# Optimization experiments

Hardware: AMD Instinct MI355X
Metric: run time of the kernel (lower is better)

## Reference

```python
import jax, jax.numpy as jnp
import numpy as np

EPS = 1e-5

def conv3x3(x, w, b=None):
    # NCHW, OIHW, stride 1, padding 1
    y = jax.lax.conv_general_dilated(x, w, (1, 1), ((1, 1), (1, 1)),
                                     dimension_numbers=('NCHW', 'OIHW', 'NCHW'))
    if b is not None:
        y = y + b[None, :, None, None]
    return y

def batchnorm(x, g, b):
    # training-mode BN (PyTorch default): biased variance over (N,H,W)
    m = x.mean((0, 2, 3), keepdims=True)
    v = x.var((0, 2, 3), keepdims=True)
    return (x - m) * jax.lax.rsqrt(v + EPS) * g[None, :, None, None] + b[None, :, None, None]

def upsample2x_align_corners(x):
    # bilinear, align_corners=True, scale_factor=2
    def lerp_axis(a, Lin, axis):
        Lout = 2 * Lin
        c = jnp.arange(Lout, dtype=a.dtype) * (Lin - 1) / (Lout - 1)
        i0 = jnp.floor(c).astype(jnp.int32)
        i1 = jnp.minimum(i0 + 1, Lin - 1)
        w = c - i0.astype(a.dtype)
        shape = [1] * a.ndim
        shape[axis] = Lout
        w = w.reshape(shape)
        return jnp.take(a, i0, axis=axis) * (1 - w) + jnp.take(a, i1, axis=axis) * w
    x = lerp_axis(x, x.shape[2], 2)
    x = lerp_axis(x, x.shape[3], 3)
    return x

def deform_sample(x, offsets):
    # torchvision DeformConv2d v1 sampling: kernel 3x3, pad 1, offsets [B,18,H,W]
    # layout: per kernel point k (row-major), channels (2k, 2k+1) = (dy, dx)
    B, C, H, W = x.shape
    K = 9
    off = offsets.reshape(B, K, 2, H, W)
    ky, kx = jnp.meshgrid(jnp.arange(3) - 1, jnp.arange(3) - 1, indexing='ij')
    ky = ky.reshape(K).astype(x.dtype)
    kx = kx.reshape(K).astype(x.dtype)
    gy = jnp.arange(H, dtype=x.dtype)[None, None, :, None]
    gx = jnp.arange(W, dtype=x.dtype)[None, None, None, :]
    py = gy + ky[None, :, None, None] + off[:, :, 0]  # [B,K,H,W]
    px = gx + kx[None, :, None, None] + off[:, :, 1]
    y0 = jnp.floor(py)
    x0 = jnp.floor(px)
    wy = (py - y0)[:, None]  # [B,1,K,H,W]
    wx = (px - x0)[:, None]
    y0i = y0.astype(jnp.int32)
    x0i = x0.astype(jnp.int32)
    x_flat = x.reshape(B, C, H * W)
    def gather(yi, xi):
        valid = ((yi >= 0) & (yi < H) & (xi >= 0) & (xi < W))
        idx = jnp.clip(yi, 0, H - 1) * W + jnp.clip(xi, 0, W - 1)  # [B,K,H,W]
        g = jnp.take_along_axis(x_flat, idx.reshape(B, 1, K * H * W), axis=2)
        return g.reshape(B, C, K, H, W) * valid[:, None].astype(x.dtype)
    v00 = gather(y0i, x0i)
    v01 = gather(y0i, x0i + 1)
    v10 = gather(y0i + 1, x0i)
    v11 = gather(y0i + 1, x0i + 1)
    return (v00 * (1 - wy) * (1 - wx) + v01 * (1 - wy) * wx
            + v10 * wy * (1 - wx) + v11 * wy * wx)

def setup_inputs() -> dict:
    key = jax.random.key(0)
    ks = jax.random.split(key, 6)
    B, in_ch, skip_ch, out_ch = 4, 256, 128, 128
    Hs, Ws = 128, 128
    x = jax.random.normal(ks[0], (B, in_ch, Hs // 2, Ws // 2), jnp.float32)
    skip = jax.random.normal(ks[1], (B, skip_ch, Hs, Ws), jnp.float32)
    cat_ch = in_ch + skip_ch
    conv1_w = jax.random.normal(ks[2], (out_ch, cat_ch, 3, 3), jnp.float32) * (2.0 / (cat_ch * 9)) ** 0.5
    off_w = jax.random.normal(ks[3], (18, out_ch, 3, 3), jnp.float32) * 0.01
    off_b = jnp.zeros((18,), jnp.float32)
    def_w = jax.random.normal(ks[4], (out_ch, out_ch, 3, 3), jnp.float32) * (2.0 / (out_ch * 9)) ** 0.5
    def_b = jnp.zeros((out_ch,), jnp.float32)
    return {
        'x': x, 'skip': skip,
        'conv1_w': conv1_w,
        'bn1_g': jnp.ones((out_ch,), jnp.float32), 'bn1_b': jnp.zeros((out_ch,), jnp.float32),
        'off_w': off_w, 'off_b': off_b,
        'def_w': def_w, 'def_b': def_b,
        'bn2_g': jnp.ones((out_ch,), jnp.float32), 'bn2_b': jnp.zeros((out_ch,), jnp.float32),
    }

def reference(x, skip, conv1_w, bn1_g, bn1_b, off_w, off_b, def_w, def_b, bn2_g, bn2_b):
    xu = upsample2x_align_corners(x)
    dh = skip.shape[2] - xu.shape[2]
    dw = skip.shape[3] - xu.shape[3]
    if dh != 0 or dw != 0:
        xu = jnp.pad(xu, ((0, 0), (0, 0), (dh // 2, dh - dh // 2), (dw // 2, dw - dw // 2)))
    cat = jnp.concatenate([skip, xu], axis=1)
    h = jax.nn.relu(batchnorm(conv3x3(cat, conv1_w), bn1_g, bn1_b))
    offsets = conv3x3(h, off_w, off_b)  # [B,18,H,W]
    sampled = deform_sample(h, offsets)  # [B,C,9,H,W]
    O = def_w.shape[0]
    y = jnp.einsum('ock,bckhw->bohw', def_w.reshape(O, def_w.shape[1], 9), sampled)
    y = y + def_b[None, :, None, None]
    return jax.nn.relu(batchnorm(y, bn2_g, bn2_b))
```

## Files before the change

kernel.cpp:

```cpp
#include <hip/hip_runtime.h>
#include <hip/hip_bf16.h>

typedef __hip_bfloat16 bf16;
typedef __bf16 bf16x8 __attribute__((ext_vector_type(8)));
typedef __bf16 bf16x4 __attribute__((ext_vector_type(4)));
typedef float  f32x4  __attribute__((ext_vector_type(4)));

constexpr int NB   = 4;
constexpr int H    = 128;
constexpr int W    = 128;
constexpr int HW   = H * W;
constexpr int NPIX = NB * HW;
constexpr int CCAT = 384;
constexpr int CSKIP= 128;
constexpr int CIN  = 256;
constexpr int CO   = 128;
constexpr int HS   = 64;
constexpr int WP   = 130;
constexpr int K1   = 3456;
constexpr int KD   = 1152;
constexpr int NBORD= 2 * WP + 2 * (WP - 2);
constexpr float EPS = 1e-5f;

__device__ __forceinline__ float b2f(bf16 v){ return __bfloat162float(v); }
__device__ __forceinline__ bf16  f2b(float v){ return __float2bfloat16(v); }

__device__ __forceinline__ void async_copy16(const void* g, void* s){
    __builtin_amdgcn_global_load_lds((const __attribute__((address_space(1))) void*)g,
                                     (__attribute__((address_space(3))) void*)s, 16, 0, 0);
}

__device__ __forceinline__ void border_yx(int p, int& y, int& x){
    if (p < WP)             { y = 0;        x = p; }
    else if (p < 2 * WP)    { y = WP - 1;   x = p - WP; }
    else if (p < 2 * WP + (WP - 2)) { y = p - 2 * WP + 1;          x = 0; }
    else                    { y = p - (2 * WP + (WP - 2)) + 1;     x = WP - 1; }
}

__global__ void k_prep(float* __restrict__ sums, bf16* __restrict__ catp,
                       bf16* __restrict__ hp){
    int i = blockIdx.x * blockDim.x + threadIdx.x;
    int stride = gridDim.x * blockDim.x;
    for (int j = i; j < 512; j += stride) sums[j] = 0.f;
    const int nCat = NB * NBORD * CCAT;
    for (int j = i; j < nCat; j += stride){
        int c = j % CCAT, r = j / CCAT, p = r % NBORD, b = r / NBORD;
        int y, x; border_yx(p, y, x);
        catp[(((size_t)b * WP + y) * WP + x) * CCAT + c] = f2b(0.f);
    }
    const int nHp = NB * NBORD * CO;
    for (int j = i; j < nHp; j += stride){
        int c = j % CO, r = j / CO, p = r % NBORD, b = r / NBORD;
        int y, x; border_yx(p, y, x);
        hp[(((size_t)b * WP + y) * WP + x) * CO + c] = f2b(0.f);
    }
}

__global__ __launch_bounds__(256) void k_build_cat2(const float* __restrict__ x,
                                                    const float* __restrict__ skip,
                                                    bf16* __restrict__ catp){
    constexpr int TS = 66;
    __shared__ bf16 tile[128 * TS];
    int t  = threadIdx.x;
    int y  = blockIdx.x % H, b = blockIdx.x / H;
    int xx = t & 127, cp = t >> 7;

    float cy = (y * 63.0f) / 127.0f;
    int   y0 = (int)cy;
    int   y1 = min(y0 + 1, HS - 1);
    float wy = cy - y0;
    float cxf = (xx * 63.0f) / 127.0f;
    int   x0 = (int)cxf;
    int   x1 = min(x0 + 1, HS - 1);
    float wx = cxf - x0;

    bf16* orow = catp + (((size_t)b * WP + y + 1) * WP + 1) * CCAT;

    for (int chunk = 0; chunk < 6; chunk++){
        int cbase = chunk * 64;
        if (chunk >= 1) __syncthreads();
        if (chunk < 2){
            const float* sb = skip + ((size_t)(b * CSKIP + cbase + cp * 32) * H + y) * W;
#pragma unroll
            for (int i = 0; i < 32; i++)
                tile[xx * TS + cp * 32 + i] = f2b(sb[(size_t)i * HW + xx]);
        } else {
            int icb = (chunk - 2) * 64 + cp * 32;
            const float* xr0 = x + ((size_t)(b * CIN + icb) * HS + y0) * HS;
            const float* xr1 = x + ((size_t)(b * CIN + icb) * HS + y1) * HS;
#pragma unroll
            for (int i = 0; i < 32; i++){
                const float* r0 = xr0 + (size_t)i * HS * HS;
                const float* r1 = xr1 + (size_t)i * HS * HS;
                float v0 = r0[x0] * (1 - wx) + r0[x1] * wx;
                float v1 = r1[x0] * (1 - wx) + r1[x1] * wx;
                tile[xx * TS + cp * 32 + i] = f2b(v0 * (1 - wy) + v1 * wy);
            }
        }
        __syncthreads();
        int cc2 = (t & 31) * 2;
        int px0 = t >> 5;
#pragma unroll
        for (int pp = 0; pp < 16; pp++){
            int px = pp * 8 + px0;
            unsigned int v = *(const unsigned int*)&tile[px * TS + cc2];
            *(unsigned int*)&orow[(size_t)px * CCAT + cbase + cc2] = v;
        }
    }
}

__global__ void k_tr_all(const float* __restrict__ w1, const float* __restrict__ wo,
                         const float* __restrict__ wd,
                         bf16* __restrict__ wt1, bf16* __restrict__ wto,
                         bf16* __restrict__ wtd){
    int i = blockIdx.x * blockDim.x + threadIdx.x;
    if (i < CO * K1){
        int k = i % K1, oc = i / K1;
        int ky = k / 1152, r = k % 1152, kx = r / 384, ic = r % 384;
        wt1[i] = f2b(w1[((oc * CCAT + ic) * 3 + ky) * 3 + kx]);
        return;
    }
    i -= CO * K1;
    if (i < 32 * KD){
        int kk = i % KD, o = i / KD;
        int ky = kk / 384, r = kk % 384, kx = r >> 7, ic = r & 127;
        wto[i] = (o < 18) ? f2b(wo[((o * CO + ic) * 3 + ky) * 3 + kx]) : f2b(0.f);
        return;
    }
    i -= 32 * KD;
    if (i < CO * KD){
        int kk = i % KD, o = i / KD;
        int kp = kk >> 7, c = kk & 127;
        wtd[i] = f2b(wd[(o * CO + c) * 9 + kp]);
    }
}

__global__ __launch_bounds__(256) void k_conv1_mfma(const bf16* __restrict__ catp,
                                                    const bf16* __restrict__ wbt,
                                                    bf16* __restrict__ hp,
                                                    float* __restrict__ sums){
    __shared__ unsigned short Ab[68 * 128];
    __shared__ unsigned short Bb[128 * 64];
    __shared__ float ps[256];
    int t = threadIdx.x;
    int l = t & 63, w = t >> 6;
    int half = blockIdx.x & 1;
    int y = (blockIdx.x >> 1) % H, b = blockIdx.x / (2 * H);
    int px0 = half * 64;

    int pr   = l >> 3;
    int koct = (l & 7) ^ pr;
    int m    = l & 15, quad = l >> 4;
    int wm   = w & 1,  wn   = w >> 1;

    f32x4 acc[2][4];
#pragma unroll
    for (int i = 0; i < 2; i++)
#pragma unroll
        for (int j = 0; j < 4; j++) acc[i][j] = f32x4{0.f, 0.f, 0.f, 0.f};

    const size_t rowStride = (size_t)WP * CCAT;
    for (int ky = 0; ky < 3; ky++){
        const bf16* Arow = catp + ((size_t)(b * WP) + y + ky) * rowStride
                         + (size_t)px0 * CCAT;
        for (int ci = 0; ci < 3; ci++){
            __syncthreads();
            for (int i = w; i < 17; i += 4){
                int G  = i * 64 + l;
                int px = G >> 4, ol = G & 15;
                int osrc = ol ^ (px & 7);
                async_copy16(Arow + (size_t)px * CCAT + ci * 128 + osrc * 8,
                             &Ab[i * 512]);
            }
            for (int kx = 0; kx < 3; kx++){
                for (int s64 = 0; s64 < 2; s64++){
                    if (kx | s64) __syncthreads();
                    int kg = ky * 1152 + kx * 384 + ci * 128 + s64 * 64;
#pragma unroll
                    for (int i = 0; i < 4; i++){
                        int ocg = w * 32 + i * 8;
                        async_copy16(wbt + (size_t)(ocg + pr) * K1 + kg + koct * 8,
                                     &Bb[ocg * 64]);
                    }
                    __syncthreads();
                    const bf16x8* ap = (const bf16x8*)Ab;
                    const bf16x8* bp = (const bf16x8*)Bb;
#pragma unroll
                    for (int ks = 0; ks < 2; ks++){
                        int s = s64 * 2 + ks;
                        bf16x8 af[2], bfr[4];
#pragma unroll
                        for (int mi = 0; mi < 2; mi++){
                            int pxk = wm * 32 + mi * 16 + m + kx;
                            af[mi] = ap[pxk * 16 + ((s * 4 + quad) ^ (pxk & 7))];
                        }
#pragma unroll
                        for (int ni = 0; ni < 4; ni++){
                            int oc = wn * 64 + ni * 16 + m;
                            bfr[ni] = bp[oc * 8 + ((ks * 4 + quad) ^ (oc & 7))];
                        }
#pragma unroll
                        for (int mi = 0; mi < 2; mi++)
#pragma unroll
                            for (int ni = 0; ni < 4; ni++)
                                acc[mi][ni] = __builtin_amdgcn_mfma_f32_16x16x32_bf16(
                                    af[mi], bfr[ni], acc[mi][ni], 0, 0, 0);
                    }
                }
            }
        }
    }
    size_t obase = (((size_t)b * WP + y + 1) * WP + 1 + px0) * CO;
#pragma unroll
    for (int mi = 0; mi < 2; mi++){
        int p0 = wm * 32 + mi * 16 + quad * 4;
#pragma unroll
        for (int ni = 0; ni < 4; ni++){
            int oc = wn * 64 + ni * 16 + m;
#pragma unroll
            for (int r = 0; r < 4; r++)
                hp[obase + (size_t)(p0 + r) * CO + oc] = f2b(acc[mi][ni][r]);
        }
    }
    ps[t] = 0.f;
    __syncthreads();
#pragma unroll
    for (int ni = 0; ni < 4; ni++){
        int ch = wn * 64 + ni * 16 + m;
        float s = 0.f, q = 0.f;
#pragma unroll
        for (int mi = 0; mi < 2; mi++)
#pragma unroll
            for (int r = 0; r < 4; r++){
                float v = acc[mi][ni][r];
                s += v; q += v * v;
            }
        s += __shfl_xor(s, 16); s += __shfl_xor(s, 32);
        q += __shfl_xor(q, 16); q += __shfl_xor(q, 32);
        if (quad == 0){
            atomicAdd(&ps[ch], s);
            atomicAdd(&ps[128 + ch], q);
        }
    }
    __syncthreads();
    if (t < 128){
        atomicAdd(&sums[t],       ps[t]);
        atomicAdd(&sums[128 + t], ps[128 + t]);
    }
}

__global__ __launch_bounds__(256) void k_bn_apply_pad(bf16* __restrict__ t,
                                                      const float* __restrict__ sums,
                                                      const float* __restrict__ g,
                                                      const float* __restrict__ bb){
    __shared__ float ssc[256];
    int tt = threadIdx.x;
    if (tt < 128){
        float mean = sums[tt] / (float)NPIX;
        float var  = sums[128 + tt] / (float)NPIX - mean * mean;
        float scale = g[tt] * rsqrtf(var + EPS);
        ssc[tt]       = scale;
        ssc[128 + tt] = bb[tt] - mean * scale;
    }
    __syncthreads();
    int i = blockIdx.x * 256 + tt;
    if (i >= NPIX * CO) return;
    int c = i & 127;
    int pix = i >> 7;
    int xw = pix & 127, yh = (pix >> 7) & 127, b = pix >> 14;
    size_t a = (((size_t)b * WP + yh + 1) * WP + xw + 1) * CO + c;
    float v = b2f(t[a]) * ssc[c] + ssc[128 + c];
    t[a] = f2b(v > 0.f ? v : 0.f);
}

__global__ __launch_bounds__(256) void k_conv_off_mfma(const bf16* __restrict__ hp,
                                                       const bf16* __restrict__ wob,
                                                       const float* __restrict__ off_b,
                                                       bf16* __restrict__ offs){
    __shared__ unsigned short Ab[132 * 128];
    __shared__ unsigned short Bb[32 * 384];
    int t = threadIdx.x, l = t & 63, w = t >> 6;
    int y = blockIdx.x % H, b = blockIdx.x / H;
    int m = l & 15, quad = l >> 4;
    int wm = w & 1, wn = w >> 1;

    f32x4 acc[4];
#pragma unroll
    for (int i = 0; i < 4; i++) acc[i] = f32x4{0.f, 0.f, 0.f, 0.f};

    const size_t rowStrideH = (size_t)WP * CO;
    for (int ky = 0; ky < 3; ky++){
        const bf16* Arow = hp + ((size_t)(b * WP) + y + ky) * rowStrideH;
        __syncthreads();
        for (int i = w; i < 33; i += 4){
            int G  = i * 64 + l;
            int px = G >> 4, ol = G & 15;
            int osrc = ol ^ (px & 7);
            async_copy16(Arow + (size_t)px * CO + osrc * 8, &Ab[i * 512]);
        }
        for (int i = w; i < 24; i += 4){
            int g  = i * 64 + l;
            int kx = g >> 9, oc = (g >> 4) & 31, ol = g & 15;
            int osrc = ol ^ (oc & 7);
            async_copy16(wob + (size_t)oc * KD + ky * 384 + kx * 128 + osrc * 8,
                         &Bb[i * 512]);
        }
        __syncthreads();
        const bf16x8* ap = (const bf16x8*)Ab;
        const bf16x8* bp = (const bf16x8*)Bb;
        for (int kx = 0; kx < 3; kx++){
#pragma unroll
            for (int s = 0; s < 4; s++){
                int oc = wn * 16 + m;
                bf16x8 bfr = bp[kx * 512 + oc * 16 + ((s * 4 + quad) ^ (oc & 7))];
#pragma unroll
                for (int mi = 0; mi < 4; mi++){
                    int pxk = wm * 64 + mi * 16 + m + kx;
                    bf16x8 af = ap[pxk * 16 + ((s * 4 + quad) ^ (pxk & 7))];
                    acc[mi] = __builtin_amdgcn_mfma_f32_16x16x32_bf16(af, bfr, acc[mi], 0, 0, 0);
                }
            }
        }
    }
    int oc = wn * 16 + m;
    if (oc < 18){
        float bias = off_b[oc];
        int rowpix = b * HW + y * W;
#pragma unroll
        for (int mi = 0; mi < 4; mi++){
            int p0 = wm * 64 + mi * 16 + quad * 4;
#pragma unroll
            for (int r = 0; r < 4; r++)
                offs[(size_t)(rowpix + p0 + r) * 18 + oc] = f2b(acc[mi][r] + bias);
        }
    }
}

__global__ __launch_bounds__(256) void k_deform_mfma(const bf16* __restrict__ hp,
                                                     const bf16* __restrict__ offs,
                                                     const bf16* __restrict__ wdb,
                                                     const float* __restrict__ def_b,
                                                     bf16* __restrict__ y,
                                                     float* __restrict__ sums){
    __shared__ unsigned short Ab[128 * 64];
    __shared__ unsigned short Bb[128 * 64];
    __shared__ int2   sc_yx[9 * 128];
    __shared__ float4 sc_w[9 * 128];
    __shared__ float  ps[256];

    int t = threadIdx.x, l = t & 63, w = t >> 6;
    int yrow = blockIdx.x % H, b = blockIdx.x / H;
    int rowpix = b * HW + yrow * W;

    for (int idx = t; idx < 9 * 128; idx += 256){
        int kp = idx >> 7, px = idx & 127;
        float dy = b2f(offs[(size_t)(rowpix + px) * 18 + 2 * kp]);
        float dx = b2f(offs[(size_t)(rowpix + px) * 18 + 2 * kp + 1]);
        float py = yrow + (kp / 3 - 1) + dy;
        float pxx = px + (kp % 3 - 1) + dx;
        float fy = floorf(py), fx = floorf(pxx);
        float wy = py - fy, wx = pxx - fx;
        int y0 = (int)fy, x0 = (int)fx;
        bool vy0 = (y0 >= 0) && (y0 < H);
        bool vy1 = (y0 + 1 >= 0) && (y0 + 1 < H);
        bool vx0 = (x0 >= 0) && (x0 < W);
        bool vx1 = (x0 + 1 >= 0) && (x0 + 1 < W);
        int y0c = min(max(y0, 0), H - 1),     y1c = min(max(y0 + 1, 0), H - 1);
        int x0c = min(max(x0, 0), W - 1),     x1c = min(max(x0 + 1, 0), W - 1);
        sc_yx[idx] = make_int2(((y0c + 1) * WP) | (((y1c + 1) * WP) << 16),
                               (x0c + 1) | ((x1c + 1) << 16));
        sc_w[idx] = make_float4((1 - wy) * (1 - wx) * (float)(vy0 && vx0),
                                (1 - wy) * wx       * (float)(vy0 && vx1),
                                wy * (1 - wx)       * (float)(vy1 && vx0),
                                wy * wx             * (float)(vy1 && vx1));
    }
    __syncthreads();

    int pr = l >> 3, koct = (l & 7) ^ pr;
    int m = l & 15, quad = l >> 4;
    int wm = w & 1, wn = w >> 1;
    int g = l >> 4, j = l & 15;

    f32x4 acc[4][4];
#pragma unroll
    for (int i = 0; i < 4; i++)
#pragma unroll
        for (int jj = 0; jj < 4; jj++) acc[i][jj] = f32x4{0.f, 0.f, 0.f, 0.f};

    const bf16* hpb = hp + (size_t)b * WP * WP * CO;

    for (int kc = 0; kc < 18; kc++){
        int kp = kc >> 1, ch = (kc & 1) * 64;
        __syncthreads();
        int kg = kp * 128 + ch;
#pragma unroll
        for (int i = 0; i < 4; i++){
            int oc = w * 32 + i * 8 + pr;
            async_copy16(wdb + (size_t)oc * KD + kg + koct * 8,
                         &Bb[(w * 32 + i * 8) * 64]);
        }
        int cb = ch + j * 4;
#pragma unroll
        for (int p = 0; p < 8; p++){
            int px = w * 32 + g * 8 + p;
            int idx = kp * 128 + px;
            int2 yx = sc_yx[idx];
            float4 w4 = sc_w[idx];
            int r0 = yx.x & 0xffff, r1 = ((unsigned)yx.x) >> 16;
            int c0 = yx.y & 0xffff, c1 = ((unsigned)yx.y) >> 16;
            const bf16* base = hpb + cb;
            bf16x4 s00 = *(const bf16x4*)(base + (size_t)(r0 + c0) * CO);
            bf16x4 s01 = *(const bf16x4*)(base + (size_t)(r0 + c1) * CO);
            bf16x4 s10 = *(const bf16x4*)(base + (size_t)(r1 + c0) * CO);
            bf16x4 s11 = *(const bf16x4*)(base + (size_t)(r1 + c1) * CO);
            bf16x4 pv;
#pragma unroll
            for (int r = 0; r < 4; r++){
                float v = w4.x * (float)s00[r] + w4.y * (float)s01[r]
                        + w4.z * (float)s10[r] + w4.w * (float)s11[r];
                pv[r] = (__bf16)v;
            }
            int oct_sw = (j >> 1) ^ (px & 7);
            *(bf16x4*)&Ab[px * 64 + oct_sw * 8 + (j & 1) * 4] = pv;
        }
        __syncthreads();
        const bf16x8* ap = (const bf16x8*)Ab;
        const bf16x8* bp = (const bf16x8*)Bb;
#pragma unroll
        for (int ks = 0; ks < 2; ks++){
            bf16x8 af[4], bfr[4];
#pragma unroll
            for (int mi = 0; mi < 4; mi++){
                int px = wm * 64 + mi * 16 + m;
                af[mi] = ap[px * 8 + ((ks * 4 + quad) ^ (px & 7))];
            }
#pragma unroll
            for (int ni = 0; ni < 4; ni++){
                int oc = wn * 64 + ni * 16 + m;
                bfr[ni] = bp[oc * 8 + ((ks * 4 + quad) ^ (oc & 7))];
            }
#pragma unroll
            for (int mi = 0; mi < 4; mi++)
#pragma unroll
                for (int ni = 0; ni < 4; ni++)
                    acc[mi][ni] = __builtin_amdgcn_mfma_f32_16x16x32_bf16(
                        af[mi], bfr[ni], acc[mi][ni], 0, 0, 0);
        }
    }
#pragma unroll
    for (int mi = 0; mi < 4; mi++){
        int p0 = wm * 64 + mi * 16 + quad * 4;
#pragma unroll
        for (int ni = 0; ni < 4; ni++){
            int oc = wn * 64 + ni * 16 + m;
            float bias = def_b[oc];
#pragma unroll
            for (int r = 0; r < 4; r++)
                y[(size_t)(rowpix + p0 + r) * CO + oc] = f2b(acc[mi][ni][r] + bias);
        }
    }
    ps[t] = 0.f;
    __syncthreads();
#pragma unroll
    for (int ni = 0; ni < 4; ni++){
        int ch = wn * 64 + ni * 16 + m;
        float bias = def_b[ch];
        float s = 0.f, q = 0.f;
#pragma unroll
        for (int mi = 0; mi < 4; mi++)
#pragma unroll
            for (int r = 0; r < 4; r++){
                float v = acc[mi][ni][r] + bias;
                s += v; q += v * v;
            }
        s += __shfl_xor(s, 16); s += __shfl_xor(s, 32);
        q += __shfl_xor(q, 16); q += __shfl_xor(q, 32);
        if (quad == 0){
            atomicAdd(&ps[ch], s);
            atomicAdd(&ps[128 + ch], q);
        }
    }
    __syncthreads();
    if (t < 128){
        atomicAdd(&sums[t],       ps[t]);
        atomicAdd(&sums[128 + t], ps[128 + t]);
    }
}

__global__ __launch_bounds__(256) void k_final(const bf16* __restrict__ yb,
                                               const float* __restrict__ sums,
                                               const float* __restrict__ g,
                                               const float* __restrict__ bb,
                                               float* __restrict__ out){
    __shared__ unsigned short tile[128 * 129];
    __shared__ float ssc[256];
    int t = threadIdx.x;
    if (t < 128){
        float mean = sums[t] / (float)NPIX;
        float var  = sums[128 + t] / (float)NPIX - mean * mean;
        float scale = g[t] * rsqrtf(var + EPS);
        ssc[t]       = scale;
        ssc[128 + t] = bb[t] - mean * scale;
    }
    int yrow = blockIdx.x % H, b = blockIdx.x / H;
    int rowbase = b * HW + yrow * W;
    const unsigned short* src = (const unsigned short*)yb;
    for (int it = 0; it < 64; it++){
        int idx = it * 256 + t;
        int c = idx & 127, px = idx >> 7;
        tile[px * 129 + c] = src[(size_t)(rowbase + px) * CO + c];
    }
    __syncthreads();
    for (int it = 0; it < 64; it++){
        int idx = it * 256 + t;
        int xw = idx & 127, o = idx >> 7;
        unsigned short u = tile[xw * 129 + o];
        float v = (float)(*(const __bf16*)&u);
        v = v * ssc[o] + ssc[128 + o];
        out[(((size_t)b * CO + o) * H + yrow) * W + xw] = v > 0.f ? v : 0.f;
    }
}

extern "C" void kernel_launch(void* const* d_in, const int* in_sizes, int n_in,
                              void* d_out, int out_size, void* d_ws, size_t ws_size,
                              hipStream_t stream){
    const float* x      = (const float*)d_in[0];
    const float* skip   = (const float*)d_in[1];
    const float* conv1w = (const float*)d_in[2];
    const float* bn1g   = (const float*)d_in[3];
    const float* bn1b   = (const float*)d_in[4];
    const float* offw   = (const float*)d_in[5];
    const float* offb   = (const float*)d_in[6];
    const float* defw   = (const float*)d_in[7];
    const float* defb   = (const float*)d_in[8];
    const float* bn2g   = (const float*)d_in[9];
    const float* bn2b   = (const float*)d_in[10];
    float* out = (float*)d_out;

    char* ws = (char*)d_ws;
    size_t off_bytes = 0;
    auto alloc = [&](size_t bytes) -> void* {
        void* p = ws + off_bytes;
        off_bytes += (bytes + 255) & ~(size_t)255;
        return p;
    };
    const size_t catp_elems = (size_t)NB * WP * WP * CCAT;
    const size_t hp_elems   = (size_t)NB * WP * WP * CO;
    bf16*  catp  = (bf16*) alloc(catp_elems * 2 + 2048);
    bf16*  hp    = (bf16*) alloc(hp_elems * 2);
    bf16*  offs  = (bf16*) alloc((size_t)NPIX * 18 * 2);
    bf16*  yb    = (bf16*) alloc((size_t)NPIX * CO * 2);
    bf16*  wbt   = (bf16*) alloc((size_t)CO * K1 * 2);
    bf16*  wob   = (bf16*) alloc((size_t)32 * KD * 2);
    bf16*  wdb   = (bf16*) alloc((size_t)CO * KD * 2);
    float* sums  = (float*)alloc(512 * 4);
    float* sums1 = sums;
    float* sums2 = sums + 256;

    k_prep<<<1024, 256, 0, stream>>>(sums, catp, hp);

    k_build_cat2<<<NB * H, 256, 0, stream>>>(x, skip, catp);

    const int ntr = CO * K1 + 32 * KD + CO * KD;
    k_tr_all<<<(ntr + 255) / 256, 256, 0, stream>>>(conv1w, offw, defw, wbt, wob, wdb);

    k_conv1_mfma<<<NB * H * 2, 256, 0, stream>>>(catp, wbt, hp, sums1);

    k_bn_apply_pad<<<(NPIX * CO + 255) / 256, 256, 0, stream>>>(hp, sums1, bn1g, bn1b);

    k_conv_off_mfma<<<NB * H, 256, 0, stream>>>(hp, wob, offb, offs);

    k_deform_mfma<<<NB * H, 256, 0, stream>>>(hp, offs, wdb, defb, yb, sums2);

    k_final<<<NB * H, 256, 0, stream>>>(yb, sums2, bn2g, bn2b, out);
}
```

Baseline: 336.1 us.

## Double-buffer conv1 MFMA LDS tiles with async prefetch and fine-grained vmcnt waits

Rewrites the conv1 implicit-GEMM main loop as one flattened 54-step pipeline. The A (activation row) and B (weight) LDS tiles are double-buffered, so the next step's tiles are fetched asynchronously while MFMAs run on the current ones. Explicit s_waitcnt vmcnt counts and raw s_barrier replace the full __syncthreads pairs, and setprio raises priority around the MFMA section. This doubles LDS usage, which may lower occupancy, and relies on hand-counted outstanding-load numbers being correct. The A loader also clamps the row index, so some waves issue duplicate copies to keep the per-wave load count uniform.

```diff
diff --git a/kernel.cpp b/kernel.cpp
--- a/kernel.cpp
+++ b/kernel.cpp
@@ -139,8 +139,8 @@
                                                     const bf16* __restrict__ wbt,
                                                     bf16* __restrict__ hp,
                                                     float* __restrict__ sums){
-    __shared__ unsigned short Ab[68 * 128];
-    __shared__ unsigned short Bb[128 * 64];
+    __shared__ unsigned short Ab[2][68 * 128];
+    __shared__ unsigned short Bb[2][128 * 64];
     __shared__ float ps[256];
     int t = threadIdx.x;
     int l = t & 63, w = t >> 6;
@@ -160,56 +160,92 @@
         for (int j = 0; j < 4; j++) acc[i][j] = f32x4{0.f, 0.f, 0.f, 0.f};
 
     const size_t rowStride = (size_t)WP * CCAT;
-    for (int ky = 0; ky < 3; ky++){
-        const bf16* Arow = catp + ((size_t)(b * WP) + y + ky) * rowStride
-                         + (size_t)px0 * CCAT;
-        for (int ci = 0; ci < 3; ci++){
-            __syncthreads();
-            for (int i = w; i < 17; i += 4){
-                int G  = i * 64 + l;
+
+    {
+        const bf16* Arow0 = catp + ((size_t)(b * WP) + y) * rowStride + (size_t)px0 * CCAT;
+#pragma unroll
+        for (int k = 0; k < 5; k++){
+            int i = min(w + k * 4, 16);
+            int G = i * 64 + l;
+            int px = G >> 4, ol = G & 15;
+            int osrc = ol ^ (px & 7);
+            async_copy16(Arow0 + (size_t)px * CCAT + osrc * 8, &Ab[0][i * 512]);
+        }
+#pragma unroll
+        for (int i = 0; i < 4; i++){
+            int ocg = w * 32 + i * 8;
+            async_copy16(wbt + (size_t)(ocg + pr) * K1 + koct * 8, &Bb[0][ocg * 64]);
+        }
+    }
+
+    for (int p = 0; p < 54; p++){
+        int g = p / 6;
+        int j = p - g * 6;
+        int s64 = j & 1, kx = j >> 1;
+
+        __builtin_amdgcn_s_barrier();
+        __builtin_amdgcn_sched_barrier(0);
+
+        if (p < 53){
+            int pn = p + 1;
+            int gn = pn / 6, jn = pn - gn * 6;
+            int kyn = gn / 3, cin = gn - kyn * 3;
+            int kgn = kyn * 1152 + (jn >> 1) * 384 + cin * 128 + (jn & 1) * 64;
+            int bufn = pn & 1;
+#pragma unroll
+            for (int i = 0; i < 4; i++){
+                int ocg = w * 32 + i * 8;
+                async_copy16(wbt + (size_t)(ocg + pr) * K1 + kgn + koct * 8,
+                             &Bb[bufn][ocg * 64]);
+            }
+        }
+        if (j == 1 && g < 8){
+            int gn = g + 1;
+            int kyn = gn / 3, cin = gn - kyn * 3;
+            const bf16* Arow2 = catp + ((size_t)(b * WP) + y + kyn) * rowStride
+                              + (size_t)px0 * CCAT + cin * 128;
+#pragma unroll
+            for (int k = 0; k < 5; k++){
+                int i = min(w + k * 4, 16);
+                int G = i * 64 + l;
                 int px = G >> 4, ol = G & 15;
                 int osrc = ol ^ (px & 7);
-                async_copy16(Arow + (size_t)px * CCAT + ci * 128 + osrc * 8,
-                             &Ab[i * 512]);
-            }
-            for (int kx = 0; kx < 3; kx++){
-                for (int s64 = 0; s64 < 2; s64++){
-                    if (kx | s64) __syncthreads();
-                    int kg = ky * 1152 + kx * 384 + ci * 128 + s64 * 64;
-#pragma unroll
-                    for (int i = 0; i < 4; i++){
-                        int ocg = w * 32 + i * 8;
-                        async_copy16(wbt + (size_t)(ocg + pr) * K1 + kg + koct * 8,
-                                     &Bb[ocg * 64]);
-                    }
-                    __syncthreads();
-                    const bf16x8* ap = (const bf16x8*)Ab;
-                    const bf16x8* bp = (const bf16x8*)Bb;
-#pragma unroll
-                    for (int ks = 0; ks < 2; ks++){
-                        int s = s64 * 2 + ks;
-                        bf16x8 af[2], bfr[4];
-#pragma unroll
-                        for (int mi = 0; mi < 2; mi++){
-                            int pxk = wm * 32 + mi * 16 + m + kx;
-                            af[mi] = ap[pxk * 16 + ((s * 4 + quad) ^ (pxk & 7))];
-                        }
-#pragma unroll
-                        for (int ni = 0; ni < 4; ni++){
-                            int oc = wn * 64 + ni * 16 + m;
-                            bfr[ni] = bp[oc * 8 + ((ks * 4 + quad) ^ (oc & 7))];
-                        }
-#pragma unroll
-                        for (int mi = 0; mi < 2; mi++)
-#pragma unroll
-                            for (int ni = 0; ni < 4; ni++)
-                                acc[mi][ni] = __builtin_amdgcn_mfma_f32_16x16x32_bf16(
-                                    af[mi], bfr[ni], acc[mi][ni], 0, 0, 0);
-                    }
-                }
-            }
-        }
-    }
+                async_copy16(Arow2 + (size_t)px * CCAT + osrc * 8, &Ab[gn & 1][i * 512]);
+            }
+        }
+        if (p == 53)                              asm volatile("s_waitcnt vmcnt(0)" ::: "memory");
+        else if ((j == 1 || j == 2) && g < 8)     asm volatile("s_waitcnt vmcnt(9)" ::: "memory");
+        else                                      asm volatile("s_waitcnt vmcnt(4)" ::: "memory");
+        __builtin_amdgcn_s_barrier();
+        __builtin_amdgcn_sched_barrier(0);
+
+        const bf16x8* ap = (const bf16x8*)&Ab[g & 1][0];
+        const bf16x8* bp = (const bf16x8*)&Bb[p & 1][0];
+        __builtin_amdgcn_s_setprio(1);
+#pragma unroll
+        for (int ks = 0; ks < 2; ks++){
+            int s = s64 * 2 + ks;
+            bf16x8 af[2], bfr[4];
+#pragma unroll
+            for (int mi = 0; mi < 2; mi++){
+                int pxk = wm * 32 + mi * 16 + m + kx;
+                af[mi] = ap[pxk * 16 + ((s * 4 + quad) ^ (pxk & 7))];
+            }
+#pragma unroll
+            for (int ni = 0; ni < 4; ni++){
+                int oc = wn * 64 + ni * 16 + m;
+                bfr[ni] = bp[oc * 8 + ((ks * 4 + quad) ^ (oc & 7))];
+            }
+#pragma unroll
+            for (int mi = 0; mi < 2; mi++)
+#pragma unroll
+                for (int ni = 0; ni < 4; ni++)
+                    acc[mi][ni] = __builtin_amdgcn_mfma_f32_16x16x32_bf16(
+                        af[mi], bfr[ni], acc[mi][ni], 0, 0, 0);
+        }
+        __builtin_amdgcn_s_setprio(0);
+    }
+
     size_t obase = (((size_t)b * WP + y + 1) * WP + 1 + px0) * CO;
 #pragma unroll
     for (int mi = 0; mi < 2; mi++){
```

New measurement: 371.7 us. 1.11x slower.

## Prepack conv1 weights in MFMA fragment order and double-buffer activation tiles

Applied to the files above, without the earlier changes.

The weight transpose kernel now writes conv1 weights pre-swizzled into the exact per-lane MFMA fragment order. The conv kernel therefore loads B fragments straight from global memory into registers, with a register double buffer one step ahead, and no longer stages them through LDS. Activation rows are double-buffered in LDS so the next (ky,ci) tile is fetched while the current one is computed. Each wave now owns 32 output channels across all 64 pixels, which cuts the syncs per K-chunk from two to one. The cost is more register pressure and weight traffic served from global/L2 by every block, and the weight buffer is over-allocated to cover the prefetch that runs past the last chunk.

```diff
diff --git a/kernel.cpp b/kernel.cpp
--- a/kernel.cpp
+++ b/kernel.cpp
@@ -115,8 +115,16 @@
                          bf16* __restrict__ wtd){
     int i = blockIdx.x * blockDim.x + threadIdx.x;
     if (i < CO * K1){
-        int k = i % K1, oc = i / K1;
-        int ky = k / 1152, r = k % 1152, kx = r / 384, ic = r % 384;
+        int e  = i & 7;
+        int l  = (i >> 3) & 63;
+        int nb = (i >> 9) & 7;
+        int ks = (i >> 12) & 1;
+        int p  = i >> 13;
+        int gp = p / 6, q = p - gp * 6;
+        int ky = gp / 3, ci = gp - ky * 3;
+        int kx = q >> 1, s64 = q & 1;
+        int oc = nb * 16 + (l & 15);
+        int ic = ci * 128 + s64 * 64 + ks * 32 + (l >> 4) * 8 + e;
         wt1[i] = f2b(w1[((oc * CCAT + ic) * 3 + ky) * 3 + kx]);
         return;
     }
@@ -139,8 +147,7 @@
                                                     const bf16* __restrict__ wbt,
                                                     bf16* __restrict__ hp,
                                                     float* __restrict__ sums){
-    __shared__ unsigned short Ab[68 * 128];
-    __shared__ unsigned short Bb[128 * 64];
+    __shared__ unsigned short Ab[2][68 * 128];
     __shared__ float ps[256];
     int t = threadIdx.x;
     int l = t & 63, w = t >> 6;
@@ -148,75 +155,104 @@
     int y = (blockIdx.x >> 1) % H, b = blockIdx.x / (2 * H);
     int px0 = half * 64;
 
-    int pr   = l >> 3;
-    int koct = (l & 7) ^ pr;
-    int m    = l & 15, quad = l >> 4;
-    int wm   = w & 1,  wn   = w >> 1;
-
-    f32x4 acc[2][4];
-#pragma unroll
-    for (int i = 0; i < 2; i++)
-#pragma unroll
-        for (int j = 0; j < 4; j++) acc[i][j] = f32x4{0.f, 0.f, 0.f, 0.f};
+    int m = l & 15, quad = l >> 4;
+
+    f32x4 acc[4][2];
+#pragma unroll
+    for (int i = 0; i < 4; i++)
+#pragma unroll
+        for (int j = 0; j < 2; j++) acc[i][j] = f32x4{0.f, 0.f, 0.f, 0.f};
 
     const size_t rowStride = (size_t)WP * CCAT;
-    for (int ky = 0; ky < 3; ky++){
-        const bf16* Arow = catp + ((size_t)(b * WP) + y + ky) * rowStride
-                         + (size_t)px0 * CCAT;
-        for (int ci = 0; ci < 3; ci++){
-            __syncthreads();
+    const char* wq = (const char*)wbt + w * 2048 + l * 16;
+
+    bf16x8 bA[2][2], bB[2][2];
+
+    {
+        const bf16* Arow = catp + ((size_t)(b * WP) + y) * rowStride + (size_t)px0 * CCAT;
+        for (int i = w; i < 17; i += 4){
+            int G = i * 64 + l;
+            int px = G >> 4, ol = G & 15;
+            int osrc = ol ^ (px & 7);
+            async_copy16(Arow + (size_t)px * CCAT + osrc * 8, &Ab[0][i * 512]);
+        }
+#pragma unroll
+        for (int ks = 0; ks < 2; ks++)
+#pragma unroll
+            for (int ni = 0; ni < 2; ni++)
+                bA[ks][ni] = *(const bf16x8*)(wq + ks * 8192 + ni * 1024);
+    }
+    __syncthreads();
+
+#pragma unroll 1
+    for (int g = 0; g < 9; g++){
+        if (g < 8){
+            int gn = g + 1;
+            int kyn = gn / 3, cin = gn - kyn * 3;
+            const bf16* Arow = catp + ((size_t)(b * WP) + y + kyn) * rowStride
+                             + (size_t)px0 * CCAT + cin * 128;
             for (int i = w; i < 17; i += 4){
-                int G  = i * 64 + l;
+                int G = i * 64 + l;
                 int px = G >> 4, ol = G & 15;
                 int osrc = ol ^ (px & 7);
-                async_copy16(Arow + (size_t)px * CCAT + ci * 128 + osrc * 8,
-                             &Ab[i * 512]);
-            }
-            for (int kx = 0; kx < 3; kx++){
-                for (int s64 = 0; s64 < 2; s64++){
-                    if (kx | s64) __syncthreads();
-                    int kg = ky * 1152 + kx * 384 + ci * 128 + s64 * 64;
-#pragma unroll
-                    for (int i = 0; i < 4; i++){
-                        int ocg = w * 32 + i * 8;
-                        async_copy16(wbt + (size_t)(ocg + pr) * K1 + kg + koct * 8,
-                                     &Bb[ocg * 64]);
-                    }
-                    __syncthreads();
-                    const bf16x8* ap = (const bf16x8*)Ab;
-                    const bf16x8* bp = (const bf16x8*)Bb;
-#pragma unroll
-                    for (int ks = 0; ks < 2; ks++){
-                        int s = s64 * 2 + ks;
-                        bf16x8 af[2], bfr[4];
-#pragma unroll
-                        for (int mi = 0; mi < 2; mi++){
-                            int pxk = wm * 32 + mi * 16 + m + kx;
-                            af[mi] = ap[pxk * 16 + ((s * 4 + quad) ^ (pxk & 7))];
-                        }
-#pragma unroll
-                        for (int ni = 0; ni < 4; ni++){
-                            int oc = wn * 64 + ni * 16 + m;
-                            bfr[ni] = bp[oc * 8 + ((ks * 4 + quad) ^ (oc & 7))];
-                        }
-#pragma unroll
-                        for (int mi = 0; mi < 2; mi++)
-#pragma unroll
-                            for (int ni = 0; ni < 4; ni++)
-                                acc[mi][ni] = __builtin_amdgcn_mfma_f32_16x16x32_bf16(
-                                    af[mi], bfr[ni], acc[mi][ni], 0, 0, 0);
-                    }
+                async_copy16(Arow + (size_t)px * CCAT + osrc * 8, &Ab[gn & 1][i * 512]);
+            }
+        }
+        const bf16x8* ap = (const bf16x8*)&Ab[g & 1][0];
+        const char* wg = wq + (size_t)g * 6 * 16384;
+#pragma unroll
+        for (int j = 0; j < 6; j++){
+            int kx = j >> 1, s64 = j & 1;
+            const char* wnx = wg + (j + 1) * 16384;
+            if (j & 1){
+#pragma unroll
+                for (int ks = 0; ks < 2; ks++)
+#pragma unroll
+                    for (int ni = 0; ni < 2; ni++)
+                        bA[ks][ni] = *(const bf16x8*)(wnx + ks * 8192 + ni * 1024);
+            } else {
+#pragma unroll
+                for (int ks = 0; ks < 2; ks++)
+#pragma unroll
+                    for (int ni = 0; ni < 2; ni++)
+                        bB[ks][ni] = *(const bf16x8*)(wnx + ks * 8192 + ni * 1024);
+            }
+#pragma unroll
+            for (int ks = 0; ks < 2; ks++){
+                int s = s64 * 2 + ks;
+                bf16x8 af[4];
+#pragma unroll
+                for (int mi = 0; mi < 4; mi++){
+                    int pxk = mi * 16 + m + kx;
+                    af[mi] = ap[pxk * 16 + ((s * 4 + quad) ^ (pxk & 7))];
                 }
-            }
-        }
-    }
+                if (j & 1){
+#pragma unroll
+                    for (int mi = 0; mi < 4; mi++)
+#pragma unroll
+                        for (int ni = 0; ni < 2; ni++)
+                            acc[mi][ni] = __builtin_amdgcn_mfma_f32_16x16x32_bf16(
+                                af[mi], bB[ks][ni], acc[mi][ni], 0, 0, 0);
+                } else {
+#pragma unroll
+                    for (int mi = 0; mi < 4; mi++)
+#pragma unroll
+                        for (int ni = 0; ni < 2; ni++)
+                            acc[mi][ni] = __builtin_amdgcn_mfma_f32_16x16x32_bf16(
+                                af[mi], bA[ks][ni], acc[mi][ni], 0, 0, 0);
+                }
+            }
+        }
+        __syncthreads();
+    }
+
     size_t obase = (((size_t)b * WP + y + 1) * WP + 1 + px0) * CO;
 #pragma unroll
-    for (int mi = 0; mi < 2; mi++){
-        int p0 = wm * 32 + mi * 16 + quad * 4;
-#pragma unroll
-        for (int ni = 0; ni < 4; ni++){
-            int oc = wn * 64 + ni * 16 + m;
+    for (int mi = 0; mi < 4; mi++){
+        int p0 = mi * 16 + quad * 4;
+#pragma unroll
+        for (int ni = 0; ni < 2; ni++){
+            int oc = w * 32 + ni * 16 + m;
 #pragma unroll
             for (int r = 0; r < 4; r++)
                 hp[obase + (size_t)(p0 + r) * CO + oc] = f2b(acc[mi][ni][r]);
@@ -225,21 +261,21 @@
     ps[t] = 0.f;
     __syncthreads();
 #pragma unroll
-    for (int ni = 0; ni < 4; ni++){
-        int ch = wn * 64 + ni * 16 + m;
-        float s = 0.f, q = 0.f;
-#pragma unroll
-        for (int mi = 0; mi < 2; mi++)
+    for (int ni = 0; ni < 2; ni++){
+        int ch = w * 32 + ni * 16 + m;
+        float s = 0.f, q2 = 0.f;
+#pragma unroll
+        for (int mi = 0; mi < 4; mi++)
 #pragma unroll
             for (int r = 0; r < 4; r++){
                 float v = acc[mi][ni][r];
-                s += v; q += v * v;
+                s += v; q2 += v * v;
             }
         s += __shfl_xor(s, 16); s += __shfl_xor(s, 32);
-        q += __shfl_xor(q, 16); q += __shfl_xor(q, 32);
+        q2 += __shfl_xor(q2, 16); q2 += __shfl_xor(q2, 32);
         if (quad == 0){
             atomicAdd(&ps[ch], s);
-            atomicAdd(&ps[128 + ch], q);
+            atomicAdd(&ps[128 + ch], q2);
         }
     }
     __syncthreads();
@@ -550,7 +586,7 @@
     bf16*  hp    = (bf16*) alloc(hp_elems * 2);
     bf16*  offs  = (bf16*) alloc((size_t)NPIX * 18 * 2);
     bf16*  yb    = (bf16*) alloc((size_t)NPIX * CO * 2);
-    bf16*  wbt   = (bf16*) alloc((size_t)CO * K1 * 2);
+    bf16*  wbt   = (bf16*) alloc((size_t)CO * K1 * 2 + 32768);
     bf16*  wob   = (bf16*) alloc((size_t)32 * KD * 2);
     bf16*  wdb   = (bf16*) alloc((size_t)CO * KD * 2);
     float* sums  = (float*)alloc(512 * 4);
```

New measurement: 333.9 us. No clear change (-0.7%).
